# Optimization experiments

Measured on AMD Instinct MI355X. Metric: run time of the kernel, lower is better.

## Reference

```python
import jax, jax.numpy as jnp
import numpy as np


def setup_inputs() -> dict:
    key = jax.random.key(0)
    k = jax.random.split(key, 5)
    C, Cb = 128, 64
    x = jax.random.normal(k[0], (8, C, 64, 64), dtype=jnp.float32)
    s_in = 1.0 / np.sqrt(C)
    s_b = 1.0 / np.sqrt(Cb)
    w_theta = jax.random.normal(k[1], (Cb, C), dtype=jnp.float32) * s_in
    w_phi = jax.random.normal(k[2], (Cb, C), dtype=jnp.float32) * s_in
    w_g = jax.random.normal(k[3], (Cb, C), dtype=jnp.float32) * s_in
    w_last = jax.random.normal(k[4], (C, Cb), dtype=jnp.float32) * s_b
    return {"x": x, "w_theta": w_theta, "w_phi": w_phi, "w_g": w_g, "w_last": w_last}


def reference(x, w_theta, w_phi, w_g, w_last):
    B, C, H, W = x.shape
    xf = x.reshape(B, C, H * W)            # [B, C, N]
    theta = jnp.einsum('kc,bcn->bkn', w_theta, xf)   # [B, Cb, N]
    phi = jnp.einsum('kc,bcn->bkn', w_phi, xf)       # [B, Cb, N]
    g = jnp.einsum('kc,bcn->bkn', w_g, xf)           # [B, Cb, N]
    # attention over spatial positions: [B, N, N]
    attn = jax.nn.softmax(jnp.einsum('bkn,bkm->bnm', theta, phi), axis=-1)
    y = jnp.einsum('bnm,bkm->bkn', attn, g)          # [B, Cb, N]
    out = jnp.einsum('ck,bkn->bcn', w_last, y).reshape(B, C, H, W)
    return out + x
```

## Files before the change

### kernel.cpp

```cpp
#include <hip/hip_runtime.h>
#include <stdint.h>

typedef _Float16 h8v __attribute__((ext_vector_type(8)));
typedef _Float16 h4v __attribute__((ext_vector_type(4)));
typedef float f4v __attribute__((ext_vector_type(4)));
typedef _Float16 f16;

#define NB 8
#define CC 128
#define CB 64
#define NN 4096
#define L2E 1.4426950408889634f

__global__ __launch_bounds__(256) void pack_w(
    const float* __restrict__ wth, const float* __restrict__ wph,
    const float* __restrict__ wg,  const float* __restrict__ wl,
    f16* __restrict__ wthp, f16* __restrict__ wphp,
    f16* __restrict__ wgp,  f16* __restrict__ wlp)
{
    const int t = blockIdx.x * 256 + threadIdx.x;
    for (int i = t; i < 8192; i += 2048){
        const int j = i & 7, lane = (i >> 3) & 63, kc = (i >> 9) & 3, ks = i >> 11;
        const int row = ks * 16 + (lane & 15);
        const int col = kc * 32 + ((lane >> 4) & 3) * 8 + j;
        wthp[i] = (f16)(wth[row * CC + col] * L2E);
        wphp[i] = (f16)(wph[row * CC + col]);
        wgp [i] = (f16)(wg [row * CC + col]);
    }
    for (int i = t; i < 8192; i += 2048){
        const int j = i & 7, lane = (i >> 3) & 63, kc = (i >> 9) & 1, cs = i >> 10;
        const int row = cs * 16 + (lane & 15);
        const int col = kc * 32 + ((lane >> 4) & 3) * 8 + j;
        wlp[i] = (f16)(wl[row * CB + col]);
    }
}

__global__ __launch_bounds__(256) void proj_kernel(
    const float* __restrict__ x, const f16* __restrict__ wthp,
    const f16* __restrict__ wphp, const f16* __restrict__ wgp,
    f16* __restrict__ thetaT, f16* __restrict__ phiT, f16* __restrict__ gbuf)
{
    __shared__ __align__(16) f16 xT[64][136];
    __shared__ __align__(16) f16 rep[4][16 * 72];
    const int b  = blockIdx.x & 7;
    const int n0 = (blockIdx.x >> 3) << 6;
    const int t  = threadIdx.x;

    #pragma unroll
    for (int i = 0; i < 8; i++){
        int v  = t + 256 * i;
        int c  = v >> 4;
        int j0 = (v & 15) << 2;
        const f4v xv = *(const f4v*)&x[((size_t)(b * CC + c)) * NN + n0 + j0];
        #pragma unroll
        for (int jj = 0; jj < 4; jj++) xT[j0 + jj][c] = (f16)xv[jj];
    }
    __syncthreads();

    const int w = t >> 6, lane = t & 63, quad = lane >> 4, l15 = lane & 15;
    const int rrow = lane >> 3, rcol = (lane & 7) * 8;

    h8v bx[4];
    #pragma unroll
    for (int kc = 0; kc < 4; kc++)
        bx[kc] = *(const h8v*)&xT[w * 16 + l15][kc * 32 + quad * 8];

    #pragma unroll
    for (int m3 = 0; m3 < 2; m3++){
        const f16* WP = (m3 == 0) ? wthp : wphp;
        f16* OUT      = (m3 == 0) ? thetaT : phiT;
        for (int ks = 0; ks < 4; ks++){
            f4v acc = {0.f, 0.f, 0.f, 0.f};
            #pragma unroll
            for (int kc = 0; kc < 4; kc++){
                const h8v af = *(const h8v*)&WP[(ks * 4 + kc) * 512 + lane * 8];
                acc = __builtin_amdgcn_mfma_f32_16x16x32_f16(af, bx[kc], acc, 0, 0, 0);
            }
            h4v pv;
            #pragma unroll
            for (int r = 0; r < 4; r++) pv[r] = (f16)acc[r];
            *(h4v*)&rep[w][l15 * 72 + ks * 16 + quad * 4] = pv;
        }
        #pragma unroll
        for (int j = 0; j < 2; j++){
            const h8v vv = *(const h8v*)&rep[w][(rrow + 8 * j) * 72 + rcol];
            *(h8v*)&OUT[((size_t)(b * NN + n0 + w * 16 + rrow + 8 * j)) * CB + rcol] = vv;
        }
    }

    h8v bw[4];
    #pragma unroll
    for (int kc = 0; kc < 4; kc++)
        bw[kc] = *(const h8v*)&wgp[(w * 4 + kc) * 512 + lane * 8];
    for (int ns = 0; ns < 4; ns++){
        f4v acc = {0.f, 0.f, 0.f, 0.f};
        #pragma unroll
        for (int kc = 0; kc < 4; kc++){
            const h8v af = *(const h8v*)&xT[ns * 16 + l15][kc * 32 + quad * 8];
            acc = __builtin_amdgcn_mfma_f32_16x16x32_f16(af, bw[kc], acc, 0, 0, 0);
        }
        h4v pv;
        #pragma unroll
        for (int r = 0; r < 4; r++) pv[r] = (f16)acc[r];
        *(h4v*)&rep[w][l15 * 72 + ns * 16 + quad * 4] = pv;
    }
    #pragma unroll
    for (int j = 0; j < 2; j++){
        const h8v vv = *(const h8v*)&rep[w][(rrow + 8 * j) * 72 + rcol];
        *(h8v*)&gbuf[((size_t)(b * CB + w * 16 + rrow + 8 * j)) * NN + n0 + rcol] = vv;
    }
}

union StageOrOut {
    struct { f16 ph[2][64 * 72]; f16 g[2][64 * 72]; } s;
    float fO[128][68];
};

__global__ __launch_bounds__(256) void attn_kernel(
    const f16* __restrict__ thetaT, const f16* __restrict__ phiT,
    const f16* __restrict__ gbuf, const f16* __restrict__ wlp,
    const float* __restrict__ x, float* __restrict__ out)
{
    __shared__ __align__(16) StageOrOut sh;
    __shared__ __align__(16) f16 plds[4][16 * 72];

    const int b  = blockIdx.x & 7;
    const int q0 = (blockIdx.x >> 3) << 6;
    const int t  = threadIdx.x;
    const int w = t >> 6, lane = t & 63, quad = lane >> 4, l15 = lane & 15;
    const int n0 = q0 + w * 16;

    const size_t trow = ((size_t)(b * NN + n0 + l15)) * CB;
    const h8v a0 = *(const h8v*)&thetaT[trow + quad * 8];
    const h8v a1 = *(const h8v*)&thetaT[trow + 32 + quad * 8];

    const int r0 = t >> 3, r1 = r0 + 32, c = (t & 7) * 8;
    const f16* pphi0 = phiT + ((size_t)(b * NN + r0)) * CB + c;
    const f16* pphi1 = phiT + ((size_t)(b * NN + r1)) * CB + c;
    const f16* pg0   = gbuf + ((size_t)(b * CB + r0)) * NN + c;
    const f16* pg1   = gbuf + ((size_t)(b * CB + r1)) * NN + c;
    const int lA = r0 * 72 + c, lB = r1 * 72 + c;

    h8v nA = *(const h8v*)pphi0;
    h8v nB = *(const h8v*)pphi1;
    h8v nC = *(const h8v*)pg0;
    h8v nD = *(const h8v*)pg1;
    *(h8v*)&sh.s.ph[0][lA] = nA;  *(h8v*)&sh.s.ph[0][lB] = nB;
    *(h8v*)&sh.s.g [0][lA] = nC;  *(h8v*)&sh.s.g [0][lB] = nD;

    float mrun = -1e30f, lrun = 0.f;
    f4v o[4];
    const f4v zf = {0.f, 0.f, 0.f, 0.f};
    #pragma unroll
    for (int tt = 0; tt < 4; tt++) o[tt] = zf;

    f16* const pw = &plds[w][0];

    for (int kb = 0; kb < 64; kb++){
        const int pb = kb & 1;
        __syncthreads();
        if (kb < 63){
            pphi0 += (size_t)64 * CB;  pphi1 += (size_t)64 * CB;
            pg0 += 64;                 pg1 += 64;
            nA = *(const h8v*)pphi0;   nB = *(const h8v*)pphi1;
            nC = *(const h8v*)pg0;     nD = *(const h8v*)pg1;
        }

        f4v s[4];
        #pragma unroll
        for (int tt = 0; tt < 4; tt++){
            const f16* pr = &sh.s.ph[pb][(tt * 16 + l15) * 72];
            const h8v pb0 = *(const h8v*)(pr + quad * 8);
            const h8v pb1 = *(const h8v*)(pr + 32 + quad * 8);
            f4v sv = zf;
            sv = __builtin_amdgcn_mfma_f32_16x16x32_f16(pb0, a0, sv, 0, 0, 0);
            sv = __builtin_amdgcn_mfma_f32_16x16x32_f16(pb1, a1, sv, 0, 0, 0);
            s[tt] = sv;
        }
        float smax = fmaxf(fmaxf(s[0][0], s[0][1]), fmaxf(s[0][2], s[0][3]));
        #pragma unroll
        for (int tt = 1; tt < 4; tt++)
            smax = fmaxf(smax, fmaxf(fmaxf(s[tt][0], s[tt][1]), fmaxf(s[tt][2], s[tt][3])));
        smax = fmaxf(smax, __shfl_xor(smax, 16));
        smax = fmaxf(smax, __shfl_xor(smax, 32));
        const float mn = fmaxf(mrun, smax);
        const float alpha = __builtin_amdgcn_exp2f(mrun - mn);
        mrun = mn;
        float lsum = 0.f;
        #pragma unroll
        for (int tt = 0; tt < 4; tt++){
            h4v pv;
            #pragma unroll
            for (int r = 0; r < 4; r++){
                float p = __builtin_amdgcn_exp2f(s[tt][r] - mn);
                lsum += p;
                pv[r] = (f16)p;
            }
            *(h4v*)&pw[l15 * 72 + tt * 16 + quad * 4] = pv;
        }
        lrun = lrun * alpha + lsum;
        #pragma unroll
        for (int tt = 0; tt < 4; tt++)
            #pragma unroll
            for (int r = 0; r < 4; r++)
                o[tt][r] *= alpha;

        const h8v pa0 = *(const h8v*)&pw[l15 * 72 + quad * 8];
        const h8v pa1 = *(const h8v*)&pw[l15 * 72 + 32 + quad * 8];

        #pragma unroll
        for (int tt = 0; tt < 4; tt++){
            const f16* gr = &sh.s.g[pb][(tt * 16 + l15) * 72];
            const h8v gb0 = *(const h8v*)(gr + quad * 8);
            const h8v gb1 = *(const h8v*)(gr + 32 + quad * 8);
            o[tt] = __builtin_amdgcn_mfma_f32_16x16x32_f16(gb0, pa0, o[tt], 0, 0, 0);
            o[tt] = __builtin_amdgcn_mfma_f32_16x16x32_f16(gb1, pa1, o[tt], 0, 0, 0);
        }

        if (kb < 63){
            const int nb = pb ^ 1;
            *(h8v*)&sh.s.ph[nb][lA] = nA;  *(h8v*)&sh.s.ph[nb][lB] = nB;
            *(h8v*)&sh.s.g [nb][lA] = nC;  *(h8v*)&sh.s.g [nb][lB] = nD;
        }
    }

    lrun += __shfl_xor(lrun, 16);
    lrun += __shfl_xor(lrun, 32);
    const float inv = 1.0f / lrun;

    #pragma unroll
    for (int tt = 0; tt < 4; tt++){
        h4v yv;
        #pragma unroll
        for (int r = 0; r < 4; r++) yv[r] = (f16)(o[tt][r] * inv);
        *(h4v*)&pw[l15 * 72 + tt * 16 + quad * 4] = yv;
    }

    __syncthreads();

    const h8v yB0 = *(const h8v*)&pw[l15 * 72 + quad * 8];
    const h8v yB1 = *(const h8v*)&pw[l15 * 72 + 32 + quad * 8];
    #pragma unroll
    for (int cs = 0; cs < 8; cs++){
        const h8v wa0 = *(const h8v*)&wlp[(cs * 2 + 0) * 512 + lane * 8];
        const h8v wa1 = *(const h8v*)&wlp[(cs * 2 + 1) * 512 + lane * 8];
        f4v acc = zf;
        acc = __builtin_amdgcn_mfma_f32_16x16x32_f16(wa0, yB0, acc, 0, 0, 0);
        acc = __builtin_amdgcn_mfma_f32_16x16x32_f16(wa1, yB1, acc, 0, 0, 0);
        #pragma unroll
        for (int r = 0; r < 4; r++)
            sh.fO[cs * 16 + quad * 4 + r][w * 16 + l15] = acc[r];
    }
    __syncthreads();

    #pragma unroll
    for (int i = 0; i < 8; i++){
        const int row = i * 16 + (t >> 4);
        const int nf  = (t & 15) * 4;
        const f4v v = *(const f4v*)&sh.fO[row][nf];
        const size_t idx = ((size_t)(b * CC + row)) * NN + q0 + nf;
        const f4v xv = *(const f4v*)&x[idx];
        f4v ov;
        #pragma unroll
        for (int r = 0; r < 4; r++) ov[r] = v[r] + xv[r];
        *(f4v*)&out[idx] = ov;
    }
}

extern "C" void kernel_launch(void* const* d_in, const int* in_sizes, int n_in,
                              void* d_out, int out_size, void* d_ws, size_t ws_size,
                              hipStream_t stream)
{
    const float* x   = (const float*)d_in[0];
    const float* wth = (const float*)d_in[1];
    const float* wph = (const float*)d_in[2];
    const float* wg  = (const float*)d_in[3];
    const float* wl  = (const float*)d_in[4];
    float* out = (float*)d_out;

    f16* thetaT = (f16*)d_ws;
    f16* phiT   = thetaT + (size_t)NB * NN * CB;
    f16* gbuf   = phiT   + (size_t)NB * NN * CB;
    f16* wthp   = gbuf   + (size_t)NB * NN * CB;
    f16* wphp   = wthp + 8192;
    f16* wgp    = wphp + 8192;
    f16* wlp    = wgp  + 8192;

    pack_w<<<8, 256, 0, stream>>>(wth, wph, wg, wl, wthp, wphp, wgp, wlp);
    proj_kernel<<<NB * 64, 256, 0, stream>>>(x, wthp, wphp, wgp, thetaT, phiT, gbuf);
    attn_kernel<<<NB * 64, 256, 0, stream>>>(thetaT, phiT, gbuf, wlp, x, out);
}
```

Baseline: 158.7 us.

## Process 32 queries per wave in attention kernel to reuse staged K/V tiles

Each wave now handles two 16-query sets (128 queries per block), so every phi/g tile staged in LDS feeds twice as many MFMAs. This halves the global and LDS traffic per query and the barrier count per unit of work. To keep LDS within budget, the output staging buffer changes from fp32 to fp16, which adds a rounding step before the residual add. The grid shrinks to 256 blocks on a 256-CU part, which lowers occupancy and latency hiding, and register pressure rises.

```diff
diff --git a/kernel.cpp b/kernel.cpp
--- a/kernel.cpp
+++ b/kernel.cpp
@@ -113,7 +113,7 @@
 
 union StageOrOut {
     struct { f16 ph[2][64 * 72]; f16 g[2][64 * 72]; } s;
-    float fO[128][68];
+    f16 fO[128][136];
 };
 
 __global__ __launch_bounds__(256) void attn_kernel(
@@ -122,17 +122,21 @@
     const float* __restrict__ x, float* __restrict__ out)
 {
     __shared__ __align__(16) StageOrOut sh;
-    __shared__ __align__(16) f16 plds[4][16 * 72];
+    __shared__ __align__(16) f16 plds[4][32 * 72];
 
     const int b  = blockIdx.x & 7;
-    const int q0 = (blockIdx.x >> 3) << 6;
+    const int q0 = (blockIdx.x >> 3) << 7;
     const int t  = threadIdx.x;
     const int w = t >> 6, lane = t & 63, quad = lane >> 4, l15 = lane & 15;
-    const int n0 = q0 + w * 16;
-
-    const size_t trow = ((size_t)(b * NN + n0 + l15)) * CB;
-    const h8v a0 = *(const h8v*)&thetaT[trow + quad * 8];
-    const h8v a1 = *(const h8v*)&thetaT[trow + 32 + quad * 8];
+    const int n0 = q0 + w * 32;
+
+    h8v a0[2], a1[2];
+    #pragma unroll
+    for (int set = 0; set < 2; set++){
+        const size_t tr = ((size_t)(b * NN + n0 + set * 16 + l15)) * CB;
+        a0[set] = *(const h8v*)&thetaT[tr + quad * 8];
+        a1[set] = *(const h8v*)&thetaT[tr + 32 + quad * 8];
+    }
 
     const int r0 = t >> 3, r1 = r0 + 32, c = (t & 7) * 8;
     const f16* pphi0 = phiT + ((size_t)(b * NN + r0)) * CB + c;
@@ -148,11 +152,13 @@
     *(h8v*)&sh.s.ph[0][lA] = nA;  *(h8v*)&sh.s.ph[0][lB] = nB;
     *(h8v*)&sh.s.g [0][lA] = nC;  *(h8v*)&sh.s.g [0][lB] = nD;
 
-    float mrun = -1e30f, lrun = 0.f;
-    f4v o[4];
+    float mrun[2] = {-1e30f, -1e30f}, lrun[2] = {0.f, 0.f};
+    f4v o[2][4];
     const f4v zf = {0.f, 0.f, 0.f, 0.f};
     #pragma unroll
-    for (int tt = 0; tt < 4; tt++) o[tt] = zf;
+    for (int set = 0; set < 2; set++)
+        #pragma unroll
+        for (int tt = 0; tt < 4; tt++) o[set][tt] = zf;
 
     f16* const pw = &plds[w][0];
 
@@ -166,55 +172,69 @@
             nC = *(const h8v*)pg0;     nD = *(const h8v*)pg1;
         }
 
-        f4v s[4];
+        f4v s[2][4];
         #pragma unroll
         for (int tt = 0; tt < 4; tt++){
             const f16* pr = &sh.s.ph[pb][(tt * 16 + l15) * 72];
             const h8v pb0 = *(const h8v*)(pr + quad * 8);
             const h8v pb1 = *(const h8v*)(pr + 32 + quad * 8);
-            f4v sv = zf;
-            sv = __builtin_amdgcn_mfma_f32_16x16x32_f16(pb0, a0, sv, 0, 0, 0);
-            sv = __builtin_amdgcn_mfma_f32_16x16x32_f16(pb1, a1, sv, 0, 0, 0);
-            s[tt] = sv;
-        }
-        float smax = fmaxf(fmaxf(s[0][0], s[0][1]), fmaxf(s[0][2], s[0][3]));
-        #pragma unroll
-        for (int tt = 1; tt < 4; tt++)
-            smax = fmaxf(smax, fmaxf(fmaxf(s[tt][0], s[tt][1]), fmaxf(s[tt][2], s[tt][3])));
-        smax = fmaxf(smax, __shfl_xor(smax, 16));
-        smax = fmaxf(smax, __shfl_xor(smax, 32));
-        const float mn = fmaxf(mrun, smax);
-        const float alpha = __builtin_amdgcn_exp2f(mrun - mn);
-        mrun = mn;
-        float lsum = 0.f;
-        #pragma unroll
-        for (int tt = 0; tt < 4; tt++){
-            h4v pv;
-            #pragma unroll
-            for (int r = 0; r < 4; r++){
-                float p = __builtin_amdgcn_exp2f(s[tt][r] - mn);
-                lsum += p;
-                pv[r] = (f16)p;
+            #pragma unroll
+            for (int set = 0; set < 2; set++){
+                f4v sv = zf;
+                sv = __builtin_amdgcn_mfma_f32_16x16x32_f16(pb0, a0[set], sv, 0, 0, 0);
+                sv = __builtin_amdgcn_mfma_f32_16x16x32_f16(pb1, a1[set], sv, 0, 0, 0);
+                s[set][tt] = sv;
             }
-            *(h4v*)&pw[l15 * 72 + tt * 16 + quad * 4] = pv;
-        }
-        lrun = lrun * alpha + lsum;
-        #pragma unroll
-        for (int tt = 0; tt < 4; tt++)
-            #pragma unroll
-            for (int r = 0; r < 4; r++)
-                o[tt][r] *= alpha;
-
-        const h8v pa0 = *(const h8v*)&pw[l15 * 72 + quad * 8];
-        const h8v pa1 = *(const h8v*)&pw[l15 * 72 + 32 + quad * 8];
+        }
+        #pragma unroll
+        for (int set = 0; set < 2; set++){
+            float smax = fmaxf(fmaxf(s[set][0][0], s[set][0][1]), fmaxf(s[set][0][2], s[set][0][3]));
+            #pragma unroll
+            for (int tt = 1; tt < 4; tt++)
+                smax = fmaxf(smax, fmaxf(fmaxf(s[set][tt][0], s[set][tt][1]),
+                                         fmaxf(s[set][tt][2], s[set][tt][3])));
+            smax = fmaxf(smax, __shfl_xor(smax, 16));
+            smax = fmaxf(smax, __shfl_xor(smax, 32));
+            const float mn = fmaxf(mrun[set], smax);
+            const float alpha = __builtin_amdgcn_exp2f(mrun[set] - mn);
+            mrun[set] = mn;
+            float lsum = 0.f;
+            #pragma unroll
+            for (int tt = 0; tt < 4; tt++){
+                h4v pv;
+                #pragma unroll
+                for (int r = 0; r < 4; r++){
+                    float p = __builtin_amdgcn_exp2f(s[set][tt][r] - mn);
+                    lsum += p;
+                    pv[r] = (f16)p;
+                }
+                *(h4v*)&pw[(set * 16 + l15) * 72 + tt * 16 + quad * 4] = pv;
+            }
+            lrun[set] = lrun[set] * alpha + lsum;
+            #pragma unroll
+            for (int tt = 0; tt < 4; tt++)
+                #pragma unroll
+                for (int r = 0; r < 4; r++)
+                    o[set][tt][r] *= alpha;
+        }
+
+        h8v pa0[2], pa1[2];
+        #pragma unroll
+        for (int set = 0; set < 2; set++){
+            pa0[set] = *(const h8v*)&pw[(set * 16 + l15) * 72 + quad * 8];
+            pa1[set] = *(const h8v*)&pw[(set * 16 + l15) * 72 + 32 + quad * 8];
+        }
 
         #pragma unroll
         for (int tt = 0; tt < 4; tt++){
             const f16* gr = &sh.s.g[pb][(tt * 16 + l15) * 72];
             const h8v gb0 = *(const h8v*)(gr + quad * 8);
             const h8v gb1 = *(const h8v*)(gr + 32 + quad * 8);
-            o[tt] = __builtin_amdgcn_mfma_f32_16x16x32_f16(gb0, pa0, o[tt], 0, 0, 0);
-            o[tt] = __builtin_amdgcn_mfma_f32_16x16x32_f16(gb1, pa1, o[tt], 0, 0, 0);
+            #pragma unroll
+            for (int set = 0; set < 2; set++){
+                o[set][tt] = __builtin_amdgcn_mfma_f32_16x16x32_f16(gb0, pa0[set], o[set][tt], 0, 0, 0);
+                o[set][tt] = __builtin_amdgcn_mfma_f32_16x16x32_f16(gb1, pa1[set], o[set][tt], 0, 0, 0);
+            }
         }
 
         if (kb < 63){
@@ -224,46 +244,53 @@
         }
     }
 
-    lrun += __shfl_xor(lrun, 16);
-    lrun += __shfl_xor(lrun, 32);
-    const float inv = 1.0f / lrun;
-
-    #pragma unroll
-    for (int tt = 0; tt < 4; tt++){
-        h4v yv;
-        #pragma unroll
-        for (int r = 0; r < 4; r++) yv[r] = (f16)(o[tt][r] * inv);
-        *(h4v*)&pw[l15 * 72 + tt * 16 + quad * 4] = yv;
+    #pragma unroll
+    for (int set = 0; set < 2; set++){
+        lrun[set] += __shfl_xor(lrun[set], 16);
+        lrun[set] += __shfl_xor(lrun[set], 32);
+        const float inv = 1.0f / lrun[set];
+        #pragma unroll
+        for (int tt = 0; tt < 4; tt++){
+            h4v yv;
+            #pragma unroll
+            for (int r = 0; r < 4; r++) yv[r] = (f16)(o[set][tt][r] * inv);
+            *(h4v*)&pw[(set * 16 + l15) * 72 + tt * 16 + quad * 4] = yv;
+        }
     }
 
     __syncthreads();
 
-    const h8v yB0 = *(const h8v*)&pw[l15 * 72 + quad * 8];
-    const h8v yB1 = *(const h8v*)&pw[l15 * 72 + 32 + quad * 8];
-    #pragma unroll
-    for (int cs = 0; cs < 8; cs++){
-        const h8v wa0 = *(const h8v*)&wlp[(cs * 2 + 0) * 512 + lane * 8];
-        const h8v wa1 = *(const h8v*)&wlp[(cs * 2 + 1) * 512 + lane * 8];
-        f4v acc = zf;
-        acc = __builtin_amdgcn_mfma_f32_16x16x32_f16(wa0, yB0, acc, 0, 0, 0);
-        acc = __builtin_amdgcn_mfma_f32_16x16x32_f16(wa1, yB1, acc, 0, 0, 0);
-        #pragma unroll
-        for (int r = 0; r < 4; r++)
-            sh.fO[cs * 16 + quad * 4 + r][w * 16 + l15] = acc[r];
+    #pragma unroll
+    for (int set = 0; set < 2; set++){
+        const h8v yB0 = *(const h8v*)&pw[(set * 16 + l15) * 72 + quad * 8];
+        const h8v yB1 = *(const h8v*)&pw[(set * 16 + l15) * 72 + 32 + quad * 8];
+        #pragma unroll
+        for (int cs = 0; cs < 8; cs++){
+            const h8v wa0 = *(const h8v*)&wlp[(cs * 2 + 0) * 512 + lane * 8];
+            const h8v wa1 = *(const h8v*)&wlp[(cs * 2 + 1) * 512 + lane * 8];
+            f4v acc = zf;
+            acc = __builtin_amdgcn_mfma_f32_16x16x32_f16(wa0, yB0, acc, 0, 0, 0);
+            acc = __builtin_amdgcn_mfma_f32_16x16x32_f16(wa1, yB1, acc, 0, 0, 0);
+            #pragma unroll
+            for (int r = 0; r < 4; r++)
+                sh.fO[cs * 16 + quad * 4 + r][w * 32 + set * 16 + l15] = (f16)acc[r];
+        }
     }
     __syncthreads();
 
     #pragma unroll
     for (int i = 0; i < 8; i++){
         const int row = i * 16 + (t >> 4);
-        const int nf  = (t & 15) * 4;
-        const f4v v = *(const f4v*)&sh.fO[row][nf];
-        const size_t idx = ((size_t)(b * CC + row)) * NN + q0 + nf;
-        const f4v xv = *(const f4v*)&x[idx];
-        f4v ov;
-        #pragma unroll
-        for (int r = 0; r < 4; r++) ov[r] = v[r] + xv[r];
-        *(f4v*)&out[idx] = ov;
+        const int jq  = (t & 15) * 8;
+        const h8v v8 = *(const h8v*)&sh.fO[row][jq];
+        const size_t idx = ((size_t)(b * CC + row)) * NN + q0 + jq;
+        const f4v x0 = *(const f4v*)&x[idx];
+        const f4v x1 = *(const f4v*)&x[idx + 4];
+        f4v o0, o1;
+        #pragma unroll
+        for (int r = 0; r < 4; r++){ o0[r] = (float)v8[r] + x0[r]; o1[r] = (float)v8[r + 4] + x1[r]; }
+        *(f4v*)&out[idx]     = o0;
+        *(f4v*)&out[idx + 4] = o1;
     }
 }
 
@@ -288,5 +315,5 @@
 
     pack_w<<<8, 256, 0, stream>>>(wth, wph, wg, wl, wthp, wphp, wgp, wlp);
     proj_kernel<<<NB * 64, 256, 0, stream>>>(x, wthp, wphp, wgp, thetaT, phiT, gbuf);
-    attn_kernel<<<NB * 64, 256, 0, stream>>>(thetaT, phiT, gbuf, wlp, x, out);
+    attn_kernel<<<NB * 32, 256, 0, stream>>>(thetaT, phiT, gbuf, wlp, x, out);
 }
```

Measured after the change: 177.3 us. +11.7%, slower.
